# Kernel tuning notes

Measured on AMD Instinct MI355X. Metric: run time of the kernel, lower is better.

The kernel has to match this reference:

```python
import jax, jax.numpy as jnp
import numpy as np

E, R, D = 4096, 64, 256
LRELU_ALPHA = 0.2

def setup_inputs() -> dict:
    key = jax.random.key(0)
    k1, k2, k3, k4, k5 = jax.random.split(key, 5)
    h = jax.random.normal(k1, (E, D), dtype=jnp.float32)
    r = jax.random.normal(k2, (R, D), dtype=jnp.float32)
    adj_agg = jax.random.normal(k3, (E, R), dtype=jnp.float32)
    lim = 1.0 / np.sqrt(D)
    W_lin = jax.random.uniform(k4, (D, 1), jnp.float32, -lim, lim)  # torch Linear(in_features, 1)
    b_lin = jax.random.uniform(k5, (1,), jnp.float32, -lim, lim)
    return {"h": h, "r": r, "adj_agg": adj_agg, "W_lin": W_lin, "b_lin": b_lin}

def reference(h, r, adj_agg, W_lin, b_lin):
    # h: (E, D), r: (R, D), adj_agg: (E, R)
    adj = jax.nn.softmax(adj_agg, axis=1)
    # (h.repeat(1,R).view(R*E,-1) * r.repeat(E,1)).view(E,R,-1) == h[e]*r[j]
    a_input = h[:, None, :] * r[None, :, :]              # (E, R, D)
    att = adj[:, :, None] * a_input                      # (E, R, D)
    att = jnp.where(att >= 0, att, LRELU_ALPHA * att)    # LeakyReLU
    att_E = jax.nn.softmax(att, axis=0)                  # softmax over entities
    att_R = jax.nn.softmax(att, axis=1)                  # softmax over relations
    # dropout is identity in eval mode
    alpha = (att_R @ W_lin + b_lin).reshape(R, E, 1)     # faithful reshape (not transpose)
    alpha = jax.nn.softmax(alpha, axis=1)
    h_prime = jnp.sum(att_E * h[:, None, :], axis=1)     # (E, D)
    r_prime = jnp.sum(att_R * r[None, :, :], axis=0)     # (R, D)
    return jax.nn.elu(h_prime), jax.nn.elu(r_prime), alpha
```

## Files before the change

kernel.cpp:

```cpp
#include <hip/hip_runtime.h>


#define EN 4096
#define RN 64
#define DN 256
#define JT 16
#define LOG2E 1.44269504088896340736f
#define CHA 8
#define CHB 8
#define ZERO_F4 ((RN*DN*2 + EN*DN*2)/4)

__device__ __forceinline__ float ex2(float x){ return __builtin_amdgcn_exp2f(x); }
__device__ __forceinline__ float rcpf(float x){ return __builtin_amdgcn_rcpf(x); }

template<int CTRL>
__device__ __forceinline__ float dpp_add(float v){
  int m = __builtin_amdgcn_update_dpp(0, __float_as_int(v), CTRL, 0xf, 0xf, true);
  return v + __int_as_float(m);
}
__device__ __forceinline__ float row16_sum(float v){
  v = dpp_add<0x111>(v);
  v = dpp_add<0x112>(v);
  v = dpp_add<0x114>(v);
  v = dpp_add<0x118>(v);
  return v;
}

__global__ __launch_bounds__(256) void k_adj(const float* __restrict__ adj,
                                             float* __restrict__ s2,
                                             float4* __restrict__ zbase){
  const int tid = threadIdx.x;
  const int gt  = blockIdx.x*256 + tid;
  for(int i = gt; i < ZERO_F4; i += (EN/4)*256)
    zbase[i] = make_float4(0.f, 0.f, 0.f, 0.f);
  const int lane = tid & 63;
  const int e = blockIdx.x*4 + (tid >> 6);
  float a = adj[e*RN + lane];
  float ev = ex2(a * LOG2E);
  float s = ev;
  #pragma unroll
  for(int off = 32; off > 0; off >>= 1) s += __shfl_xor(s, off, 64);
  s2[e*RN + lane] = ev * (LOG2E * rcpf(s));
}

__global__ __launch_bounds__(256,4) void kA(const float* __restrict__ h,
                                            const float* __restrict__ r,
                                            const float* __restrict__ s2,
                                            float* __restrict__ lRg,
                                            float* __restrict__ lE){
  const int d  = threadIdx.x;
  const int e0 = (blockIdx.x >> 2) * CHA;
  const int j0 = (blockIdx.x & 3) * JT;
  __shared__ float s2s[CHA*JT];
  if(d < CHA*JT) s2s[d] = s2[(e0 + (d >> 4))*RN + j0 + (d & 15)];
  __syncthreads();

  float lR[CHA];
  #pragma unroll
  for(int ee = 0; ee < CHA; ee++) lR[ee] = 0.f;

  float rcol[JT], lEacc[JT];
  #pragma unroll
  for(int jj = 0; jj < JT; jj++){ rcol[jj] = r[(j0+jj)*DN + d]; lEacc[jj] = 0.f; }
  #pragma unroll
  for(int ee = 0; ee < CHA; ee++){
    const float he = h[(e0+ee)*DN + d];
    #pragma unroll
    for(int jj = 0; jj < JT; jj++){
      float t  = s2s[ee*JT + jj] * he * rcol[jj];
      float ev = ex2(fmaxf(t, 0.2f*t));
      lR[ee]   += ev;
      lEacc[jj] += ev;
    }
  }
  #pragma unroll
  for(int jj = 0; jj < JT; jj++) atomicAdd(&lE[(j0+jj)*DN + d], lEacc[jj]);
  #pragma unroll
  for(int ee = 0; ee < CHA; ee++) atomicAdd(&lRg[(e0+ee)*DN + d], lR[ee]);
}

__global__ __launch_bounds__(256,4) void kB(const float* __restrict__ h,
                                            const float* __restrict__ r,
                                            const float* __restrict__ s2,
                                            const float* __restrict__ lRg,
                                            const float* __restrict__ lE,
                                            const float* __restrict__ W,
                                            float* __restrict__ alog,
                                            float* __restrict__ racc_g,
                                            float* __restrict__ sEg){
  const int tid  = threadIdx.x;
  const int lane = tid & 63;
  const int grp  = tid >> 4;
  const int e0   = (blockIdx.x >> 2) * CHB;
  const int j0   = (blockIdx.x & 3) * JT;
  __shared__ float s2s[CHB*JT];
  __shared__ float apart[CHB*16*20];
  if(tid < CHB*JT) s2s[tid] = s2[(e0 + (tid >> 4))*RN + j0 + (tid & 15)];
  __syncthreads();

  const float wd = W[tid];
  float sE[CHB];
  #pragma unroll
  for(int ee = 0; ee < CHB; ee++) sE[ee] = 0.f;

  float rcol[JT], ile[JT], rAcc[JT];
  #pragma unroll
  for(int jj = 0; jj < JT; jj++){
    const int j = j0 + jj;
    rcol[jj] = r[j*DN + tid];
    ile[jj]  = rcpf(lE[j*DN + tid]);
    rAcc[jj] = 0.f;
  }
  for(int ee = 0; ee < CHB; ee++){
    const int e = e0 + ee;
    const float he = h[e*DN + tid];
    const float il = rcpf(lRg[e*DN + tid]);
    const float u  = il * wd;
    #pragma unroll
    for(int jg = 0; jg < JT/4; jg++){
      float4 st;
      #pragma unroll
      for(int jj4 = 0; jj4 < 4; jj4++){
        const int jj = jg*4 + jj4;
        float t  = s2s[ee*JT + jj] * he * rcol[jj];
        float ev = ex2(fmaxf(t, 0.2f*t));
        rAcc[jj] = fmaf(ev, il, rAcc[jj]);
        sE[ee]   = fmaf(ev, ile[jj], sE[ee]);
        float rs = row16_sum(ev * u);
        if(jj4==0) st.x = rs; else if(jj4==1) st.y = rs;
        else if(jj4==2) st.z = rs; else st.w = rs;
      }
      if((lane & 15) == 15){
        *reinterpret_cast<float4*>(&apart[(ee*16 + grp)*20 + jg*4]) = st;
      }
    }
  }
  __syncthreads();
  if(tid < CHB*JT){
    const int ee = tid >> 4, jj = tid & 15;
    float sum = 0.f;
    #pragma unroll
    for(int g = 0; g < 16; g++) sum += apart[(ee*16 + g)*20 + jj];
    alog[(e0+ee)*RN + j0 + jj] = sum;
  }
  #pragma unroll
  for(int jj = 0; jj < JT; jj++) atomicAdd(&racc_g[(j0+jj)*DN + tid], rAcc[jj]);
  #pragma unroll
  for(int ee = 0; ee < CHB; ee++) atomicAdd(&sEg[(e0+ee)*DN + tid], sE[ee]);
}

__global__ __launch_bounds__(256) void kTail(const float* __restrict__ h,
                                             const float* __restrict__ sEg,
                                             const float* __restrict__ alog,
                                             const float* __restrict__ r,
                                             const float* __restrict__ racc,
                                             float* __restrict__ hout,
                                             float* __restrict__ rout,
                                             float* __restrict__ aout){
  const int b = blockIdx.x, tid = threadIdx.x;
  {
    const int i = b*256 + tid;
    float hp = h[i] * sEg[i];
    hout[i] = hp > 0.f ? hp : (ex2(hp*LOG2E) - 1.0f);
  }
  if(b < RN){
    const int i = b*DN + tid;
    float v = r[i] * racc[i];
    rout[i] = v > 0.f ? v : (ex2(v*LOG2E) - 1.0f);

    const float* __restrict__ row = alog + b*EN;
    float exv[16]; float s = 0.f;
    #pragma unroll
    for(int k = 0; k < 16; k++){
      float v2 = ex2(row[k*256 + tid] * LOG2E);
      exv[k] = v2; s += v2;
    }
    #pragma unroll
    for(int off = 32; off > 0; off >>= 1) s += __shfl_xor(s, off, 64);
    __shared__ float wsum[4];
    if((tid & 63) == 0) wsum[tid>>6] = s;
    __syncthreads();
    float inv = 1.0f / (wsum[0] + wsum[1] + wsum[2] + wsum[3]);
    float* __restrict__ orow = aout + b*EN;
    #pragma unroll
    for(int k = 0; k < 16; k++) orow[k*256 + tid] = exv[k] * inv;
  }
}

extern "C" void kernel_launch(void* const* d_in, const int* in_sizes, int n_in,
                              void* d_out, int out_size, void* d_ws, size_t ws_size,
                              hipStream_t stream){
  (void)in_sizes; (void)n_in; (void)out_size; (void)ws_size;
  const float* h   = (const float*)d_in[0];
  const float* r   = (const float*)d_in[1];
  const float* adj = (const float*)d_in[2];
  const float* W   = (const float*)d_in[3];

  float* ws   = (float*)d_ws;
  float* s2   = ws;
  float* lE   = s2 + EN*RN;
  float* racc = lE + RN*DN;
  float* lRg  = racc + RN*DN;
  float* sEg  = lRg + EN*DN;
  float* alog = sEg + EN*DN;

  float* hout = (float*)d_out;
  float* rout = hout + EN*DN;
  float* aout = rout + RN*DN;

  k_adj<<<EN/4,      256, 0, stream>>>(adj, s2, (float4*)lE);
  kA   <<<EN/CHA*4,  256, 0, stream>>>(h, r, s2, lRg, lE);
  kB   <<<EN/CHB*4,  256, 0, stream>>>(h, r, s2, lRg, lE, W, alog, racc, sEg);
  kTail<<<EN*DN/256, 256, 0, stream>>>(h, sEg, alog, r, racc, hout, rout, aout);
}
```

Baseline: 168.8 us.

## Fuse adjacency softmax into kA and use transpose-reduce shuffles in kB

Drops the separate k_adj kernel. Each kA block now computes the softmax rows of adj it needs, writes its slice of s2 to global for kB, and zeroes the racc/sEg accumulators. The lE/lRg accumulators are cleared with a hipMemsetAsync, and the workspace order is changed so each zeroed region is contiguous. In kB, the per-j DPP row-16 reductions become a butterfly transpose-reduce over xor shuffles (8, 4, 2, 1), so each lane ends up holding one column sum, which cuts shuffle work. The costs are a memset launch that replaces the kernel launch and softmax work repeated four times per entity row.

```diff
diff --git a/kernel.cpp b/kernel.cpp
--- a/kernel.cpp
+++ b/kernel.cpp
@@ -8,51 +8,46 @@
 #define LOG2E 1.44269504088896340736f
 #define CHA 8
 #define CHB 8
-#define ZERO_F4 ((RN*DN*2 + EN*DN*2)/4)
+#define GRIDAB ((EN/CHA)*4)
+#define NZ4 ((RN*DN + EN*DN)/4)
 
 __device__ __forceinline__ float ex2(float x){ return __builtin_amdgcn_exp2f(x); }
 __device__ __forceinline__ float rcpf(float x){ return __builtin_amdgcn_rcpf(x); }
 
-template<int CTRL>
-__device__ __forceinline__ float dpp_add(float v){
-  int m = __builtin_amdgcn_update_dpp(0, __float_as_int(v), CTRL, 0xf, 0xf, true);
-  return v + __int_as_float(m);
-}
-__device__ __forceinline__ float row16_sum(float v){
-  v = dpp_add<0x111>(v);
-  v = dpp_add<0x112>(v);
-  v = dpp_add<0x114>(v);
-  v = dpp_add<0x118>(v);
-  return v;
-}
-
-__global__ __launch_bounds__(256) void k_adj(const float* __restrict__ adj,
-                                             float* __restrict__ s2,
-                                             float4* __restrict__ zbase){
-  const int tid = threadIdx.x;
-  const int gt  = blockIdx.x*256 + tid;
-  for(int i = gt; i < ZERO_F4; i += (EN/4)*256)
-    zbase[i] = make_float4(0.f, 0.f, 0.f, 0.f);
-  const int lane = tid & 63;
-  const int e = blockIdx.x*4 + (tid >> 6);
-  float a = adj[e*RN + lane];
-  float ev = ex2(a * LOG2E);
-  float s = ev;
-  #pragma unroll
-  for(int off = 32; off > 0; off >>= 1) s += __shfl_xor(s, off, 64);
-  s2[e*RN + lane] = ev * (LOG2E * rcpf(s));
-}
-
 __global__ __launch_bounds__(256,4) void kA(const float* __restrict__ h,
                                             const float* __restrict__ r,
-                                            const float* __restrict__ s2,
+                                            const float* __restrict__ adj,
+                                            float* __restrict__ s2g,
                                             float* __restrict__ lRg,
-                                            float* __restrict__ lE){
+                                            float* __restrict__ lE,
+                                            float4* __restrict__ zb){
   const int d  = threadIdx.x;
-  const int e0 = (blockIdx.x >> 2) * CHA;
-  const int j0 = (blockIdx.x & 3) * JT;
+  const int b  = blockIdx.x;
+  const int e0 = (b >> 2) * CHA;
+  const int j0 = (b & 3) * JT;
+
+  for(int i = b*256 + d; i < NZ4; i += GRIDAB*256)
+    zb[i] = make_float4(0.f, 0.f, 0.f, 0.f);
+
   __shared__ float s2s[CHA*JT];
-  if(d < CHA*JT) s2s[d] = s2[(e0 + (d >> 4))*RN + j0 + (d & 15)];
+  {
+    const int w = d >> 6, lane = d & 63;
+    #pragma unroll
+    for(int rr2 = 0; rr2 < 2; rr2++){
+      const int row = rr2*4 + w;
+      float a  = adj[(e0 + row)*RN + lane];
+      float ev = ex2(a * LOG2E);
+      float s  = ev;
+      #pragma unroll
+      for(int off = 32; off > 0; off >>= 1) s += __shfl_xor(s, off, 64);
+      float val = ev * (LOG2E * rcpf(s));
+      const unsigned lj = (unsigned)(lane - j0);
+      if(lj < 16u){
+        s2s[row*JT + (int)lj] = val;
+        s2g[(e0 + row)*RN + j0 + (int)lj] = val;
+      }
+    }
+  }
   __syncthreads();
 
   float lR[CHA];
@@ -91,8 +86,9 @@
   const int tid  = threadIdx.x;
   const int lane = tid & 63;
   const int grp  = tid >> 4;
-  const int e0   = (blockIdx.x >> 2) * CHB;
-  const int j0   = (blockIdx.x & 3) * JT;
+  const int b    = blockIdx.x;
+  const int e0   = (b >> 2) * CHB;
+  const int j0   = (b & 3) * JT;
   __shared__ float s2s[CHB*JT];
   __shared__ float apart[CHB*16*20];
   if(tid < CHB*JT) s2s[tid] = s2[(e0 + (tid >> 4))*RN + j0 + (tid & 15)];
@@ -111,28 +107,50 @@
     ile[jj]  = rcpf(lE[j*DN + tid]);
     rAcc[jj] = 0.f;
   }
+  const bool l8 = (lane & 8) != 0;
+  const bool l4 = (lane & 4) != 0;
+  const bool l2 = (lane & 2) != 0;
+  const bool l1 = (lane & 1) != 0;
   for(int ee = 0; ee < CHB; ee++){
     const int e = e0 + ee;
     const float he = h[e*DN + tid];
     const float il = rcpf(lRg[e*DN + tid]);
     const float u  = il * wd;
-    #pragma unroll
-    for(int jg = 0; jg < JT/4; jg++){
-      float4 st;
-      #pragma unroll
-      for(int jj4 = 0; jj4 < 4; jj4++){
-        const int jj = jg*4 + jj4;
-        float t  = s2s[ee*JT + jj] * he * rcol[jj];
-        float ev = ex2(fmaxf(t, 0.2f*t));
-        rAcc[jj] = fmaf(ev, il, rAcc[jj]);
-        sE[ee]   = fmaf(ev, ile[jj], sE[ee]);
-        float rs = row16_sum(ev * u);
-        if(jj4==0) st.x = rs; else if(jj4==1) st.y = rs;
-        else if(jj4==2) st.z = rs; else st.w = rs;
-      }
-      if((lane & 15) == 15){
-        *reinterpret_cast<float4*>(&apart[(ee*16 + grp)*20 + jg*4]) = st;
-      }
+    float aw[JT];
+    #pragma unroll
+    for(int jj = 0; jj < JT; jj++){
+      float t  = s2s[ee*JT + jj] * he * rcol[jj];
+      float ev = ex2(fmaxf(t, 0.2f*t));
+      rAcc[jj] = fmaf(ev, il, rAcc[jj]);
+      sE[ee]   = fmaf(ev, ile[jj], sE[ee]);
+      aw[jj]   = ev * u;
+    }
+    float b8[8];
+    #pragma unroll
+    for(int i = 0; i < 8; i++){
+      float send = l8 ? aw[i] : aw[i+8];
+      float got  = __shfl_xor(send, 8, 64);
+      b8[i] = (l8 ? aw[i+8] : aw[i]) + got;
+    }
+    float c4[4];
+    #pragma unroll
+    for(int i = 0; i < 4; i++){
+      float send = l4 ? b8[i] : b8[i+4];
+      float got  = __shfl_xor(send, 4, 64);
+      c4[i] = (l4 ? b8[i+4] : b8[i]) + got;
+    }
+    float d2[2];
+    #pragma unroll
+    for(int i = 0; i < 2; i++){
+      float send = l2 ? c4[i] : c4[i+2];
+      float got  = __shfl_xor(send, 2, 64);
+      d2[i] = (l2 ? c4[i+2] : c4[i]) + got;
+    }
+    {
+      float send = l1 ? d2[0] : d2[1];
+      float got  = __shfl_xor(send, 1, 64);
+      float f0   = (l1 ? d2[1] : d2[0]) + got;
+      apart[(ee*16 + grp)*20 + (lane & 15)] = f0;
     }
   }
   __syncthreads();
@@ -199,17 +217,17 @@
   float* ws   = (float*)d_ws;
   float* s2   = ws;
   float* lE   = s2 + EN*RN;
-  float* racc = lE + RN*DN;
-  float* lRg  = racc + RN*DN;
-  float* sEg  = lRg + EN*DN;
+  float* lRg  = lE + RN*DN;
+  float* racc = lRg + EN*DN;
+  float* sEg  = racc + RN*DN;
   float* alog = sEg + EN*DN;
 
   float* hout = (float*)d_out;
   float* rout = hout + EN*DN;
   float* aout = rout + RN*DN;
 
-  k_adj<<<EN/4,      256, 0, stream>>>(adj, s2, (float4*)lE);
-  kA   <<<EN/CHA*4,  256, 0, stream>>>(h, r, s2, lRg, lE);
-  kB   <<<EN/CHB*4,  256, 0, stream>>>(h, r, s2, lRg, lE, W, alog, racc, sEg);
-  kTail<<<EN*DN/256, 256, 0, stream>>>(h, sEg, alog, r, racc, hout, rout, aout);
-}
+  hipMemsetAsync(lE, 0, size_t(RN*DN + EN*DN)*sizeof(float), stream);
+  kA   <<<GRIDAB,     256, 0, stream>>>(h, r, adj, s2, lRg, lE, (float4*)racc);
+  kB   <<<GRIDAB,     256, 0, stream>>>(h, r, s2, lRg, lE, W, alog, racc, sEg);
+  kTail<<<EN*DN/256,  256, 0, stream>>>(h, sEg, alog, r, racc, hout, rout, aout);
+}
```

Measured after the change: 264.5 us. 1.57x slower.

## Process multiple entity chunks per block to amortize relation-column atomics

Applied to the files above, without the earlier changes.

Each block in kA and kB now loops over SLAB=4 consecutive chunks of entities, keeping the relation-side accumulators (lEacc, rAcc) in registers across chunks. This cuts the per-column atomicAdds to lE and racc by a factor of four, and reduces the redundant loads and reciprocals of r and lE. The grid shrinks fourfold to 512 blocks, which lowers parallelism, and kB gains an extra barrier per chunk.

```diff
diff --git a/kernel.cpp b/kernel.cpp
--- a/kernel.cpp
+++ b/kernel.cpp
@@ -8,6 +8,8 @@
 #define LOG2E 1.44269504088896340736f
 #define CHA 8
 #define CHB 8
+#define SLAB 4
+#define GRIDS ((EN/(CHA*SLAB))*4)
 #define ZERO_F4 ((RN*DN*2 + EN*DN*2)/4)
 
 __device__ __forceinline__ float ex2(float x){ return __builtin_amdgcn_exp2f(x); }
@@ -48,35 +50,42 @@
                                             const float* __restrict__ s2,
                                             float* __restrict__ lRg,
                                             float* __restrict__ lE){
-  const int d  = threadIdx.x;
-  const int e0 = (blockIdx.x >> 2) * CHA;
-  const int j0 = (blockIdx.x & 3) * JT;
-  __shared__ float s2s[CHA*JT];
-  if(d < CHA*JT) s2s[d] = s2[(e0 + (d >> 4))*RN + j0 + (d & 15)];
+  const int d   = threadIdx.x;
+  const int e00 = (blockIdx.x >> 2) * (CHA*SLAB);
+  const int j0  = (blockIdx.x & 3) * JT;
+  __shared__ float s2s[SLAB*CHA*JT];
+  #pragma unroll
+  for(int k = 0; k < SLAB*CHA*JT/256; k++){
+    const int idx = k*256 + d;
+    s2s[idx] = s2[(e00 + (idx >> 4))*RN + j0 + (idx & 15)];
+  }
   __syncthreads();
 
-  float lR[CHA];
-  #pragma unroll
-  for(int ee = 0; ee < CHA; ee++) lR[ee] = 0.f;
-
   float rcol[JT], lEacc[JT];
   #pragma unroll
   for(int jj = 0; jj < JT; jj++){ rcol[jj] = r[(j0+jj)*DN + d]; lEacc[jj] = 0.f; }
-  #pragma unroll
-  for(int ee = 0; ee < CHA; ee++){
-    const float he = h[(e0+ee)*DN + d];
-    #pragma unroll
-    for(int jj = 0; jj < JT; jj++){
-      float t  = s2s[ee*JT + jj] * he * rcol[jj];
-      float ev = ex2(fmaxf(t, 0.2f*t));
-      lR[ee]   += ev;
-      lEacc[jj] += ev;
-    }
+
+  for(int sc = 0; sc < SLAB; sc++){
+    const int e0 = e00 + sc*CHA;
+    float lR[CHA];
+    #pragma unroll
+    for(int ee = 0; ee < CHA; ee++) lR[ee] = 0.f;
+    #pragma unroll
+    for(int ee = 0; ee < CHA; ee++){
+      const float he = h[(e0+ee)*DN + d];
+      #pragma unroll
+      for(int jj = 0; jj < JT; jj++){
+        float t  = s2s[(sc*CHA+ee)*JT + jj] * he * rcol[jj];
+        float ev = ex2(fmaxf(t, 0.2f*t));
+        lR[ee]   += ev;
+        lEacc[jj] += ev;
+      }
+    }
+    #pragma unroll
+    for(int ee = 0; ee < CHA; ee++) atomicAdd(&lRg[(e0+ee)*DN + d], lR[ee]);
   }
   #pragma unroll
   for(int jj = 0; jj < JT; jj++) atomicAdd(&lE[(j0+jj)*DN + d], lEacc[jj]);
-  #pragma unroll
-  for(int ee = 0; ee < CHA; ee++) atomicAdd(&lRg[(e0+ee)*DN + d], lR[ee]);
 }
 
 __global__ __launch_bounds__(256,4) void kB(const float* __restrict__ h,
@@ -91,18 +100,18 @@
   const int tid  = threadIdx.x;
   const int lane = tid & 63;
   const int grp  = tid >> 4;
-  const int e0   = (blockIdx.x >> 2) * CHB;
+  const int e00  = (blockIdx.x >> 2) * (CHB*SLAB);
   const int j0   = (blockIdx.x & 3) * JT;
-  __shared__ float s2s[CHB*JT];
+  __shared__ float s2s[SLAB*CHB*JT];
   __shared__ float apart[CHB*16*20];
-  if(tid < CHB*JT) s2s[tid] = s2[(e0 + (tid >> 4))*RN + j0 + (tid & 15)];
+  #pragma unroll
+  for(int k = 0; k < SLAB*CHB*JT/256; k++){
+    const int idx = k*256 + tid;
+    s2s[idx] = s2[(e00 + (idx >> 4))*RN + j0 + (idx & 15)];
+  }
   __syncthreads();
 
   const float wd = W[tid];
-  float sE[CHB];
-  #pragma unroll
-  for(int ee = 0; ee < CHB; ee++) sE[ee] = 0.f;
-
   float rcol[JT], ile[JT], rAcc[JT];
   #pragma unroll
   for(int jj = 0; jj < JT; jj++){
@@ -111,42 +120,50 @@
     ile[jj]  = rcpf(lE[j*DN + tid]);
     rAcc[jj] = 0.f;
   }
-  for(int ee = 0; ee < CHB; ee++){
-    const int e = e0 + ee;
-    const float he = h[e*DN + tid];
-    const float il = rcpf(lRg[e*DN + tid]);
-    const float u  = il * wd;
-    #pragma unroll
-    for(int jg = 0; jg < JT/4; jg++){
-      float4 st;
+
+  for(int sc = 0; sc < SLAB; sc++){
+    const int e0 = e00 + sc*CHB;
+    float sE[CHB];
+    #pragma unroll
+    for(int ee = 0; ee < CHB; ee++) sE[ee] = 0.f;
+    for(int ee = 0; ee < CHB; ee++){
+      const int e = e0 + ee;
+      const float he = h[e*DN + tid];
+      const float il = rcpf(lRg[e*DN + tid]);
+      const float u  = il * wd;
       #pragma unroll
-      for(int jj4 = 0; jj4 < 4; jj4++){
-        const int jj = jg*4 + jj4;
-        float t  = s2s[ee*JT + jj] * he * rcol[jj];
-        float ev = ex2(fmaxf(t, 0.2f*t));
-        rAcc[jj] = fmaf(ev, il, rAcc[jj]);
-        sE[ee]   = fmaf(ev, ile[jj], sE[ee]);
-        float rs = row16_sum(ev * u);
-        if(jj4==0) st.x = rs; else if(jj4==1) st.y = rs;
-        else if(jj4==2) st.z = rs; else st.w = rs;
+      for(int jg = 0; jg < JT/4; jg++){
+        float4 st;
+        #pragma unroll
+        for(int jj4 = 0; jj4 < 4; jj4++){
+          const int jj = jg*4 + jj4;
+          float t  = s2s[(sc*CHB+ee)*JT + jj] * he * rcol[jj];
+          float ev = ex2(fmaxf(t, 0.2f*t));
+          rAcc[jj] = fmaf(ev, il, rAcc[jj]);
+          sE[ee]   = fmaf(ev, ile[jj], sE[ee]);
+          float rs = row16_sum(ev * u);
+          if(jj4==0) st.x = rs; else if(jj4==1) st.y = rs;
+          else if(jj4==2) st.z = rs; else st.w = rs;
+        }
+        if((lane & 15) == 15){
+          *reinterpret_cast<float4*>(&apart[(ee*16 + grp)*20 + jg*4]) = st;
+        }
       }
-      if((lane & 15) == 15){
-        *reinterpret_cast<float4*>(&apart[(ee*16 + grp)*20 + jg*4]) = st;
-      }
-    }
-  }
-  __syncthreads();
-  if(tid < CHB*JT){
-    const int ee = tid >> 4, jj = tid & 15;
-    float sum = 0.f;
-    #pragma unroll
-    for(int g = 0; g < 16; g++) sum += apart[(ee*16 + g)*20 + jj];
-    alog[(e0+ee)*RN + j0 + jj] = sum;
+    }
+    __syncthreads();
+    if(tid < CHB*JT){
+      const int ee = tid >> 4, jj = tid & 15;
+      float sum = 0.f;
+      #pragma unroll
+      for(int g = 0; g < 16; g++) sum += apart[(ee*16 + g)*20 + jj];
+      alog[(e0+ee)*RN + j0 + jj] = sum;
+    }
+    #pragma unroll
+    for(int ee = 0; ee < CHB; ee++) atomicAdd(&sEg[(e0+ee)*DN + tid], sE[ee]);
+    __syncthreads();
   }
   #pragma unroll
   for(int jj = 0; jj < JT; jj++) atomicAdd(&racc_g[(j0+jj)*DN + tid], rAcc[jj]);
-  #pragma unroll
-  for(int ee = 0; ee < CHB; ee++) atomicAdd(&sEg[(e0+ee)*DN + tid], sE[ee]);
 }
 
 __global__ __launch_bounds__(256) void kTail(const float* __restrict__ h,
@@ -209,7 +226,7 @@
   float* aout = rout + RN*DN;
 
   k_adj<<<EN/4,      256, 0, stream>>>(adj, s2, (float4*)lE);
-  kA   <<<EN/CHA*4,  256, 0, stream>>>(h, r, s2, lRg, lE);
-  kB   <<<EN/CHB*4,  256, 0, stream>>>(h, r, s2, lRg, lE, W, alog, racc, sEg);
+  kA   <<<GRIDS,     256, 0, stream>>>(h, r, s2, lRg, lE);
+  kB   <<<GRIDS,     256, 0, stream>>>(h, r, s2, lRg, lE, W, alog, racc, sEg);
   kTail<<<EN*DN/256, 256, 0, stream>>>(h, sEg, alog, r, racc, hout, rout, aout);
 }
```

Result: slower. 200.6 us (+18.9%).
